# Optimization experiments

Hardware: AMD Instinct MI355X
Metric: run time of the kernel (lower is better)

Reference implementation:

```python
import jax, jax.numpy as jnp
import numpy as np

# norse LIF/LI defaults
DT = 1e-3
TAU_SYN_INV = 200.0
TAU_MEM_INV = 100.0
V_TH = 1.0
V_LEAK = 0.0
V_RESET = 0.0
ALPHA = 100.0  # SuperSpike surrogate slope ('super' method)
N_CLASSES = 10


@jax.custom_vjp
def spike(x):
    # heaviside forward, SuperSpike surrogate backward
    return (x > 0).astype(x.dtype)

def _spike_fwd(x):
    return spike(x), x

def _spike_bwd(x, g):
    return (g / (ALPHA * jnp.abs(x) + 1.0) ** 2,)

spike.defvjp(_spike_fwd, _spike_bwd)


def conv2d(x, w, b):
    y = jax.lax.conv_general_dilated(x, w, (1, 1), 'VALID',
                                     dimension_numbers=('NCHW', 'OIHW', 'NCHW'))
    return y + b[None, :, None, None]


def maxpool2(x):
    return jax.lax.reduce_window(x, -jnp.inf, jax.lax.max,
                                 (1, 1, 2, 2), (1, 1, 2, 2), 'VALID')


def lif_step(inp, v, i):
    # norse lif_feed_forward_step
    v_dec = v + DT * TAU_MEM_INV * ((V_LEAK - v) + i)
    i_dec = i * (1.0 - DT * TAU_SYN_INV)
    z = spike(v_dec - V_TH)
    v_new = (1.0 - z) * v_dec + z * V_RESET
    i_new = i_dec + inp
    return z, v_new, i_new


def setup_inputs() -> dict:
    key = jax.random.key(0)
    ks = jax.random.split(key, 9)
    T, B, C, H = 32, 32, 1, 64
    feats = 13 * 13 * 32  # 5408
    return {
        'x': jax.random.normal(ks[0], (T, B, C, H, H), jnp.float32),
        'conv1_w': jax.random.normal(ks[1], (16, 1, 5, 5), jnp.float32) * 0.2,
        'conv1_b': jax.random.normal(ks[2], (16,), jnp.float32) * 0.1,
        'conv2_w': jax.random.normal(ks[3], (32, 16, 5, 5), jnp.float32) * 0.05,
        'conv2_b': jax.random.normal(ks[4], (32,), jnp.float32) * 0.1,
        'fc1_w': jax.random.normal(ks[5], (500, feats), jnp.float32) * 0.02,
        'fc1_b': jax.random.normal(ks[6], (500,), jnp.float32) * 0.1,
        'out_w': jax.random.normal(ks[7], (10, 500), jnp.float32) * 0.06,
    }


def reference(x, conv1_w, conv1_b, conv2_w, conv2_b, fc1_w, fc1_b, out_w):
    B = x.shape[1]
    zeros = lambda s: jnp.zeros(s, x.dtype)
    init = ((zeros((B, 16, 60, 60)), zeros((B, 16, 60, 60))),
            (zeros((B, 32, 26, 26)), zeros((B, 32, 26, 26))),
            (zeros((B, 500)), zeros((B, 500))),
            (zeros((B, N_CLASSES)), zeros((B, N_CLASSES))))

    def step(state, xt):
        (v0, i0), (v1, i1), (v2, i2), (vo, io) = state
        z = conv2d(xt, conv1_w, conv1_b)                     # [B,16,60,60]
        z, v0, i0 = lif_step(z, v0, i0)
        z = maxpool2(z)                                      # [B,16,30,30]
        z = N_CLASSES * conv2d(z, conv2_w, conv2_b)          # [B,32,26,26]
        z, v1, i1 = lif_step(z, v1, i1)
        z = maxpool2(z).reshape(B, -1)                       # [B,5408]
        z = z @ fc1_w.T + fc1_b                              # [B,500]
        z, v2, i2 = lif_step(z, v2, i2)
        zr = jax.nn.relu(z)
        # LI (non-spiking) linear readout cell: norse li_step, no bias
        v_out = vo + DT * TAU_MEM_INV * ((V_LEAK - vo) + io)
        io = io * (1.0 - DT * TAU_SYN_INV) + zr @ out_w.T
        return ((v0, i0), (v1, i1), (v2, i2), (v_out, io)), v_out

    _, voltages = jax.lax.scan(step, init, x)
    return voltages  # [T, B, n_classes]
```

## Files before the change

kernel.cpp:

```cpp
#include <hip/hip_runtime.h>


#define T_STEPS 32

typedef __bf16 bf16x8 __attribute__((ext_vector_type(8)));
typedef float f32x16 __attribute__((ext_vector_type(16)));
typedef int i32x4 __attribute__((ext_vector_type(4)));

__device__ __forceinline__ int xcd_swz(int orig, int nwg) {
    const int q = nwg >> 3, r = nwg & 7;
    const int xcd = orig & 7, idx = orig >> 3;
    return (xcd < r ? xcd * (q + 1) : r * (q + 1) + (xcd - r) * q) + idx;
}

__global__ __launch_bounds__(256) void k_tr(
    const float* __restrict__ x, float* __restrict__ xT)
{
    const int y = blockIdx.x, t = blockIdx.y;
    const int tid = threadIdx.x;
    __shared__ float tile[32][65];

    const int lx = tid & 63, bg = tid >> 6;
    #pragma unroll
    for (int p = 0; p < 8; ++p) {
        const int b = bg + p * 4;
        tile[b][lx] = x[((size_t)(t * 32 + b) * 64 + y) * 64 + lx];
    }
    __syncthreads();
    const int wb = tid & 31, xg = tid >> 5;
    #pragma unroll
    for (int p = 0; p < 8; ++p) {
        const int xx = xg + p * 8;
        xT[((size_t)(t * 64 + y) * 64 + xx) * 32 + wb] = tile[wb][xx];
    }
}

__global__ __launch_bounds__(256) void k1_conv1(
    const float* __restrict__ xT,
    const float* __restrict__ w1,
    const float* __restrict__ b1,
    unsigned short* __restrict__ zp1c)
{
    const int pos = xcd_swz(blockIdx.x, 900);
    const int py = pos / 30, px = pos % 30;
    const int y0 = 2 * py, x0 = 2 * px;
    const int tid = threadIdx.x;
    const int b = tid & 31, slot = tid >> 5;

    __shared__ float ws[400];
    __shared__ float win[1152];
    for (int i = tid; i < 400; i += 256) ws[i] = w1[i];
    const float bias0 = b1[slot], bias1 = b1[slot + 8];
    const float* __restrict__ wc0 = ws + slot * 25;
    const float* __restrict__ wc1 = ws + (slot + 8) * 25;

    float v[2][4] = {{0.f,0.f,0.f,0.f},{0.f,0.f,0.f,0.f}};
    float cu[2][4] = {{0.f,0.f,0.f,0.f},{0.f,0.f,0.f,0.f}};

    const size_t obase = (size_t)pos * 256 + (slot >> 1) * 64 + b * 2 + (slot & 1);

    for (int t = 0; t < T_STEPS; ++t) {
        __syncthreads();
        {
            const float4* __restrict__ src0 =
                (const float4*)(xT + ((size_t)(t * 64 + y0) * 64 + x0) * 32);
            float4* __restrict__ dst = (float4*)win;
            for (int i = tid; i < 288; i += 256) {
                const int r = i / 48, j = i - r * 48;
                dst[r * 48 + j] = src0[r * 512 + j];
            }
        }
        __syncthreads();

        float xr[36];
        #pragma unroll
        for (int rc = 0; rc < 36; ++rc) xr[rc] = win[rc * 32 + b];

        float acc0[4] = {0.f, 0.f, 0.f, 0.f};
        float acc1[4] = {0.f, 0.f, 0.f, 0.f};
        #pragma unroll
        for (int ky = 0; ky < 5; ++ky) {
            #pragma unroll
            for (int kx = 0; kx < 5; ++kx) {
                const float w0 = wc0[ky * 5 + kx];
                const float w1v = wc1[ky * 5 + kx];
                const float e00 = xr[ky * 6 + kx];
                const float e01 = xr[ky * 6 + kx + 1];
                const float e10 = xr[(ky + 1) * 6 + kx];
                const float e11 = xr[(ky + 1) * 6 + kx + 1];
                acc0[0] = fmaf(w0, e00, acc0[0]);
                acc0[1] = fmaf(w0, e01, acc0[1]);
                acc0[2] = fmaf(w0, e10, acc0[2]);
                acc0[3] = fmaf(w0, e11, acc0[3]);
                acc1[0] = fmaf(w1v, e00, acc1[0]);
                acc1[1] = fmaf(w1v, e01, acc1[1]);
                acc1[2] = fmaf(w1v, e10, acc1[2]);
                acc1[3] = fmaf(w1v, e11, acc1[3]);
            }
        }

        #pragma unroll
        for (int half = 0; half < 2; ++half) {
            const float* acc = half ? acc1 : acc0;
            const float bias = half ? bias1 : bias0;
            float zmax = 0.f;
            #pragma unroll
            for (int q = 0; q < 4; ++q) {
                const float inp = acc[q] + bias;
                const float vv = v[half][q], cur = cu[half][q];
                const float vd = vv + 0.1f * (cur - vv);
                const float id = 0.8f * cur;
                const float z = (vd - 1.0f > 0.0f) ? 1.0f : 0.0f;
                v[half][q] = (z > 0.f) ? 0.f : vd;
                cu[half][q] = id + inp;
                zmax = fmaxf(zmax, z);
            }
            zp1c[(size_t)t * 460800 + (size_t)half * 230400 + obase] =
                (unsigned short)(__float_as_uint(zmax) >> 16);
        }
    }
}

__global__ __launch_bounds__(256) void k2w_split(
    const float* __restrict__ w2, unsigned short* __restrict__ wsplit)
{
    const int i = blockIdx.x * 256 + threadIdx.x;
    if (i >= 12800) return;
    const int co = i / 400, rest = i % 400;
    const int ci = rest / 25, tap = rest % 25;
    const float w = w2[i];
    const unsigned wb = __float_as_uint(w);
    const unsigned hi = wb & 0xFFFF0000u;
    const float r1 = w - __uint_as_float(hi);
    const unsigned mid = __float_as_uint(r1) & 0xFFFF0000u;
    const float r2 = r1 - __uint_as_float(mid);
    const unsigned lo = __float_as_uint(r2) & 0xFFFF0000u;
    const int base = (tap * 32 + co) * 16 + ci;
    wsplit[base]         = (unsigned short)(hi >> 16);
    wsplit[12800 + base] = (unsigned short)(mid >> 16);
    wsplit[25600 + base] = (unsigned short)(lo >> 16);
}

__global__ __launch_bounds__(256, 2) void k2a_mfma(
    const unsigned* __restrict__ zp1c,
    const unsigned short* __restrict__ wsplit,
    float* __restrict__ raw)
{
    __shared__ i32x4 wlds[4800];
    const int tid = threadIdx.x;
    for (int i = tid; i < 4800; i += 256)
        wlds[i] = ((const i32x4*)wsplit)[i];
    __syncthreads();

    const int w = tid >> 6, l = tid & 63;
    const int task = xcd_swz(blockIdx.x, 1352) * 4 + w;
    const int t = task / 169, pg = task % 169;
    const int py = pg / 13, px = pg % 13;
    const int b = l & 31, cig = l >> 5;
    const int abase = (l & 31) * 2 + cig;

    const unsigned* __restrict__ zt =
        zp1c + (size_t)(t * 2 + cig) * 115200 + ((2 * py) * 30 + 2 * px) * 128 + b;

    f32x16 accA, accB, accC, accD;
    #pragma unroll
    for (int r = 0; r < 16; ++r) { accA[r] = 0.f; accB[r] = 0.f; accC[r] = 0.f; accD[r] = 0.f; }

    #pragma unroll
    for (int wy = 0; wy < 6; ++wy) {
        i32x4 bw[6];
        #pragma unroll
        for (int wx = 0; wx < 6; ++wx) {
            const unsigned* __restrict__ c = zt + (wy * 30 + wx) * 128;
            bw[wx][0] = (int)c[0];
            bw[wx][1] = (int)c[32];
            bw[wx][2] = (int)c[64];
            bw[wx][3] = (int)c[96];
        }
        if (wy <= 4) {
            #pragma unroll
            for (int sp = 0; sp < 3; ++sp) {
                #pragma unroll
                for (int kx = 0; kx < 5; ++kx) {
                    const int tap = wy * 5 + kx;
                    const bf16x8 A = __builtin_bit_cast(bf16x8, wlds[(sp * 25 + tap) * 64 + abase]);
                    accA = __builtin_amdgcn_mfma_f32_32x32x16_bf16(
                        A, __builtin_bit_cast(bf16x8, bw[kx]),     accA, 0, 0, 0);
                    accB = __builtin_amdgcn_mfma_f32_32x32x16_bf16(
                        A, __builtin_bit_cast(bf16x8, bw[kx + 1]), accB, 0, 0, 0);
                }
            }
        }
        if (wy >= 1) {
            #pragma unroll
            for (int sp = 0; sp < 3; ++sp) {
                #pragma unroll
                for (int kx = 0; kx < 5; ++kx) {
                    const int tap = (wy - 1) * 5 + kx;
                    const bf16x8 A = __builtin_bit_cast(bf16x8, wlds[(sp * 25 + tap) * 64 + abase]);
                    accC = __builtin_amdgcn_mfma_f32_32x32x16_bf16(
                        A, __builtin_bit_cast(bf16x8, bw[kx]),     accC, 0, 0, 0);
                    accD = __builtin_amdgcn_mfma_f32_32x32x16_bf16(
                        A, __builtin_bit_cast(bf16x8, bw[kx + 1]), accD, 0, 0, 0);
                }
            }
        }
    }

    float* __restrict__ rp = raw + (size_t)(t * 169 + pg) * 4096 + b;
    const int hi = l >> 5;
    #pragma unroll
    for (int r = 0; r < 16; ++r) {
        const int row = (r & 3) + 8 * (r >> 2) + 4 * hi;
        rp[row * 32]        = accA[r];
        rp[1024 + row * 32] = accB[r];
        rp[2048 + row * 32] = accC[r];
        rp[3072 + row * 32] = accD[r];
    }
}

__global__ __launch_bounds__(256) void k2b_lifpool(
    const float* __restrict__ raw,
    const float* __restrict__ b2,
    float* __restrict__ zp2a)
{
    const int bid = blockIdx.x;
    const int pg = bid >> 2, cog = bid & 3;
    const int tid = threadIdx.x;
    const int co = cog * 8 + (tid >> 5), b = tid & 31;
    const float bias = b2[co];
    const float* __restrict__ rp = raw + (size_t)pg * 4096 + co * 32 + b;

    float v0=0.f,v1=0.f,v2=0.f,v3=0.f, c0=0.f,c1=0.f,c2=0.f,c3=0.f;
    for (int t = 0; t < T_STEPS; ++t) {
        const float* __restrict__ r = rp + (size_t)t * 692224;
        float zm = 0.f;
        { const float inp = 10.f*(r[0]    + bias); const float vd = v0 + 0.1f*(c0-v0);
          const float z = (vd-1.f>0.f)?1.f:0.f; v0 = (z>0.f)?0.f:vd; c0 = 0.8f*c0 + inp;
          zm = fmaxf(zm, z); }
        { const float inp = 10.f*(r[1024] + bias); const float vd = v1 + 0.1f*(c1-v1);
          const float z = (vd-1.f>0.f)?1.f:0.f; v1 = (z>0.f)?0.f:vd; c1 = 0.8f*c1 + inp;
          zm = fmaxf(zm, z); }
        { const float inp = 10.f*(r[2048] + bias); const float vd = v2 + 0.1f*(c2-v2);
          const float z = (vd-1.f>0.f)?1.f:0.f; v2 = (z>0.f)?0.f:vd; c2 = 0.8f*c2 + inp;
          zm = fmaxf(zm, z); }
        { const float inp = 10.f*(r[3072] + bias); const float vd = v3 + 0.1f*(c3-v3);
          const float z = (vd-1.f>0.f)?1.f:0.f; v3 = (z>0.f)?0.f:vd; c3 = 0.8f*c3 + inp;
          zm = fmaxf(zm, z); }
        zp2a[(size_t)t * 173056 + (co * 169 + pg) * 32 + b] = zm;
    }
}

__global__ __launch_bounds__(256) void k3w_split(
    const float* __restrict__ fw, unsigned short* __restrict__ wf)
{
    const int gid = blockIdx.x * 256 + threadIdx.x;
    const int l = gid & 31;
    const int ks = (gid >> 5) % 338;
    const int nt = gid / 10816;
    const int n = nt * 32 + l;

    unsigned hipk[8], midpk[8], lopk[8];
    #pragma unroll
    for (int p = 0; p < 8; ++p) {
        unsigned h[2], m[2], o[2];
        #pragma unroll
        for (int e = 0; e < 2; ++e) {
            const float w = (n < 500) ? fw[(size_t)n * 5408 + ks * 16 + 2 * p + e] : 0.f;
            const unsigned wb = __float_as_uint(w);
            const unsigned hi = wb & 0xFFFF0000u;
            const float r1 = w - __uint_as_float(hi);
            const unsigned mid = __float_as_uint(r1) & 0xFFFF0000u;
            const float r2 = r1 - __uint_as_float(mid);
            h[e] = hi >> 16; m[e] = mid >> 16; o[e] = __float_as_uint(r2) >> 16;
        }
        hipk[p]  = h[0] | (h[1] << 16);
        midpk[p] = m[0] | (m[1] << 16);
        lopk[p]  = o[0] | (o[1] << 16);
    }

    i32x4* __restrict__ wv = (i32x4*)wf;
    const int base = (nt * 338 + ks) * 64 + l * 2;
    i32x4 a, bq;
    a[0]=(int)hipk[0];a[1]=(int)hipk[1];a[2]=(int)hipk[2];a[3]=(int)hipk[3];
    bq[0]=(int)hipk[4];bq[1]=(int)hipk[5];bq[2]=(int)hipk[6];bq[3]=(int)hipk[7];
    wv[base] = a; wv[base + 1] = bq;
    a[0]=(int)midpk[0];a[1]=(int)midpk[1];a[2]=(int)midpk[2];a[3]=(int)midpk[3];
    bq[0]=(int)midpk[4];bq[1]=(int)midpk[5];bq[2]=(int)midpk[6];bq[3]=(int)midpk[7];
    wv[base + 346112] = a; wv[base + 346113] = bq;
    a[0]=(int)lopk[0];a[1]=(int)lopk[1];a[2]=(int)lopk[2];a[3]=(int)lopk[3];
    bq[0]=(int)lopk[4];bq[1]=(int)lopk[5];bq[2]=(int)lopk[6];bq[3]=(int)lopk[7];
    wv[base + 692224] = a; wv[base + 692225] = bq;
}

__global__ __launch_bounds__(256) void zpack(
    const float* __restrict__ zp2a, unsigned short* __restrict__ zb)
{
    const int gid = blockIdx.x * 256 + threadIdx.x;
    const int b = gid & 31;
    const int kh = (gid >> 5) & 1;
    const int rest = gid >> 6;
    const int ks = rest % 338;
    const int t = rest / 338;

    const float* __restrict__ zp = zp2a + (size_t)t * 173056 + (ks * 16 + kh * 8) * 32 + b;
    i32x4 pk;
    #pragma unroll
    for (int p = 0; p < 4; ++p) {
        const unsigned v0 = __float_as_uint(zp[(2 * p) * 32]) >> 16;
        const unsigned v1 = __float_as_uint(zp[(2 * p + 1) * 32]) & 0xFFFF0000u;
        pk[p] = (int)(v0 | v1);
    }
    ((i32x4*)zb)[gid] = pk;
}

__global__ __launch_bounds__(256) void k3_mfma(
    const unsigned short* __restrict__ wf,
    const unsigned short* __restrict__ zb,
    float* __restrict__ part)
{
    const int wgid = xcd_swz(blockIdx.x, 416);
    const int ntg = wgid / 52, rest = wgid % 52;
    const int kc = rest >> 2, cgg = rest & 3;
    const int tid = threadIdx.x;
    const int w = tid >> 6, l = tid & 63;
    const int nt = ntg * 2 + (w >> 1);
    const int cg = cgg * 2 + (w & 1);
    const int lo5 = l & 31, hi1 = l >> 5;

    const i32x4* __restrict__ wv = (const i32x4*)wf;
    const i32x4* __restrict__ zv = (const i32x4*)zb;

    f32x16 acc0, acc1, acc2, acc3;
    #pragma unroll
    for (int r = 0; r < 16; ++r) { acc0[r]=0.f; acc1[r]=0.f; acc2[r]=0.f; acc3[r]=0.f; }

    const int ks0 = kc * 26;
    #pragma unroll 2
    for (int kk = 0; kk < 26; ++kk) {
        const int ks = ks0 + kk;
        const int ab = (nt * 338 + ks) * 64 + lo5 * 2 + hi1;
        const bf16x8 A0 = __builtin_bit_cast(bf16x8, wv[ab]);
        const bf16x8 A1 = __builtin_bit_cast(bf16x8, wv[ab + 346112]);
        const bf16x8 A2 = __builtin_bit_cast(bf16x8, wv[ab + 692224]);
        const int b0 = (((cg * 4) * 338 + ks) * 2 + hi1) * 32 + lo5;
        const bf16x8 B0 = __builtin_bit_cast(bf16x8, zv[b0]);
        const bf16x8 B1 = __builtin_bit_cast(bf16x8, zv[b0 + 21632]);
        const bf16x8 B2 = __builtin_bit_cast(bf16x8, zv[b0 + 43264]);
        const bf16x8 B3 = __builtin_bit_cast(bf16x8, zv[b0 + 64896]);
        acc0 = __builtin_amdgcn_mfma_f32_32x32x16_bf16(A0, B0, acc0, 0, 0, 0);
        acc1 = __builtin_amdgcn_mfma_f32_32x32x16_bf16(A0, B1, acc1, 0, 0, 0);
        acc2 = __builtin_amdgcn_mfma_f32_32x32x16_bf16(A0, B2, acc2, 0, 0, 0);
        acc3 = __builtin_amdgcn_mfma_f32_32x32x16_bf16(A0, B3, acc3, 0, 0, 0);
        acc0 = __builtin_amdgcn_mfma_f32_32x32x16_bf16(A1, B0, acc0, 0, 0, 0);
        acc1 = __builtin_amdgcn_mfma_f32_32x32x16_bf16(A1, B1, acc1, 0, 0, 0);
        acc2 = __builtin_amdgcn_mfma_f32_32x32x16_bf16(A1, B2, acc2, 0, 0, 0);
        acc3 = __builtin_amdgcn_mfma_f32_32x32x16_bf16(A1, B3, acc3, 0, 0, 0);
        acc0 = __builtin_amdgcn_mfma_f32_32x32x16_bf16(A2, B0, acc0, 0, 0, 0);
        acc1 = __builtin_amdgcn_mfma_f32_32x32x16_bf16(A2, B1, acc1, 0, 0, 0);
        acc2 = __builtin_amdgcn_mfma_f32_32x32x16_bf16(A2, B2, acc2, 0, 0, 0);
        acc3 = __builtin_amdgcn_mfma_f32_32x32x16_bf16(A2, B3, acc3, 0, 0, 0);
    }

    float* __restrict__ pp = part + ((size_t)(kc * 512 + nt * 32)) * 1024 + cg * 128 + lo5;
    #pragma unroll
    for (int r = 0; r < 16; ++r) {
        const int row = (r & 3) + 8 * (r >> 2) + 4 * hi1;
        pp[row * 1024]      = acc0[r];
        pp[row * 1024 + 32] = acc1[r];
        pp[row * 1024 + 64] = acc2[r];
        pp[row * 1024 + 96] = acc3[r];
    }
}

__global__ __launch_bounds__(256) void k3b_lif(
    const float* __restrict__ part,
    const float* __restrict__ fb,
    float* __restrict__ za)
{
    const int idx = blockIdx.x * 256 + threadIdx.x;
    if (idx >= 16000) return;
    const int n = idx >> 5, b = idx & 31;
    const float bias = fb[n];

    float v = 0.f, cu = 0.f;
    for (int t = 0; t < T_STEPS; ++t) {
        float s = 0.f;
        #pragma unroll
        for (int p = 0; p < 13; ++p)
            s += part[(size_t)p * 524288 + n * 1024 + t * 32 + b];
        s += bias;

        const float vd = v + 0.1f * (cu - v);
        const float id = 0.8f * cu;
        const float z = (vd - 1.0f > 0.0f) ? 1.0f : 0.0f;
        v = (z > 0.f) ? 0.f : vd;
        cu = id + s;
        za[(size_t)t * 16000 + idx] = z;
    }
}

__global__ __launch_bounds__(256) void k4_dot(
    const float* __restrict__ za,
    const float* __restrict__ ow,
    float* __restrict__ dota)
{
    const int c = blockIdx.x, t = blockIdx.y;
    const int tid = threadIdx.x;
    const int b = tid & 31, nc = tid >> 5;
    const float* __restrict__ wr = ow + c * 500;
    const float* __restrict__ zt = za + (size_t)t * 16000;

    float acc = 0.f;
    for (int j = 0; j < 63; ++j) {
        const int n = nc * 63 + j;
        if (n < 500) acc = fmaf(zt[n * 32 + b], wr[n], acc);
    }

    __shared__ float red[256];
    red[tid] = acc;
    __syncthreads();
    if (tid < 32) {
        float dot = 0.f;
        #pragma unroll
        for (int q = 0; q < 8; ++q) dot += red[q * 32 + tid];
        dota[((size_t)t * 10 + c) * 32 + tid] = dot;
    }
}

__global__ __launch_bounds__(320) void k5_li(
    const float* __restrict__ dota,
    float* __restrict__ outp)
{
    const int tid = threadIdx.x;
    if (tid >= 320) return;
    const int c = tid / 32, b = tid & 31;

    float vo = 0.f, io = 0.f;
    for (int t = 0; t < T_STEPS; ++t) {
        const float vout = vo + 0.1f * (io - vo);
        outp[t * 320 + b * 10 + c] = vout;
        vo = vout;
        io = 0.8f * io + dota[(t * 10 + c) * 32 + b];
    }
}

extern "C" void kernel_launch(void* const* d_in, const int* in_sizes, int n_in,
                              void* d_out, int out_size, void* d_ws, size_t ws_size,
                              hipStream_t stream) {
    const float* x  = (const float*)d_in[0];
    const float* w1 = (const float*)d_in[1];
    const float* b1 = (const float*)d_in[2];
    const float* w2 = (const float*)d_in[3];
    const float* b2 = (const float*)d_in[4];
    const float* fw = (const float*)d_in[5];
    const float* fb = (const float*)d_in[6];
    const float* ow = (const float*)d_in[7];
    float* out = (float*)d_out;
    float* ws = (float*)d_ws;

    size_t off = 0;
    float* zp1a = ws + off; off += 14745600;
    float* zp2a = ws + off; off += 5537792;
    float* za   = ws + off; off += 512000;
    float* dota = ws + off; off += 10240;
    unsigned short* wsplit = (unsigned short*)(ws + off); off += 19200;
    float* big  = ws + off; off += 22151168;

    float* xT       = big;
    float* conv2raw = big;
    float* part     = big;
    unsigned short* zp1c = (unsigned short*)zp1a;
    unsigned short* zb = (unsigned short*)zp1a;
    unsigned short* wf = (unsigned short*)(zp1a + 4194304);

    k2w_split<<<50, 256, 0, stream>>>(w2, wsplit);
    k_tr     <<<dim3(64, 32), 256, 0, stream>>>(x, xT);
    k1_conv1 <<<900, 256, 0, stream>>>(xT, w1, b1, zp1c);
    k2a_mfma <<<1352, 256, 0, stream>>>((const unsigned*)zp1c, wsplit, conv2raw);
    k2b_lifpool<<<676, 256, 0, stream>>>(conv2raw, b2, zp2a);
    k3w_split<<<676, 256, 0, stream>>>(fw, wf);
    zpack    <<<2704, 256, 0, stream>>>(zp2a, zb);
    k3_mfma  <<<416, 256, 0, stream>>>(wf, zb, part);
    k3b_lif  <<<63, 256, 0, stream>>>(part, fb, za);
    k4_dot   <<<dim3(10, 32), 256, 0, stream>>>(za, ow, dota);
    k5_li    <<<1, 320, 0, stream>>>(dota, out);
}
```

Before: 236.2 us.

## Batch conv1 timesteps in LDS, keep weights in registers, fuse zpack into lifpool

conv1 now loads an 8-timestep input window into shared memory at once, stored in a transposed per-batch layout so that float4 reads can be used. This cuts the number of barriers per block from 64 to 8. Filter weights are held in registers instead of shared memory. The separate zpack kernel is removed: k2b_lifpool writes bf16 spikes directly in the packed layout that k3_mfma expects, which avoids one launch and an fp32 intermediate round trip. The trade-off is more registers and LDS per block in conv1, plus scattered 2-byte stores in lifpool.

```diff
diff --git a/kernel.cpp b/kernel.cpp
--- a/kernel.cpp
+++ b/kernel.cpp
@@ -47,76 +47,97 @@
     const int tid = threadIdx.x;
     const int b = tid & 31, slot = tid >> 5;
 
-    __shared__ float ws[400];
-    __shared__ float win[1152];
-    for (int i = tid; i < 400; i += 256) ws[i] = w1[i];
+    __shared__ float win[8 * 32 * 36];
+
+    float wreg[2][25];
+    #pragma unroll
+    for (int k = 0; k < 25; ++k) {
+        wreg[0][k] = w1[slot * 25 + k];
+        wreg[1][k] = w1[(slot + 8) * 25 + k];
+    }
     const float bias0 = b1[slot], bias1 = b1[slot + 8];
-    const float* __restrict__ wc0 = ws + slot * 25;
-    const float* __restrict__ wc1 = ws + (slot + 8) * 25;
 
     float v[2][4] = {{0.f,0.f,0.f,0.f},{0.f,0.f,0.f,0.f}};
     float cu[2][4] = {{0.f,0.f,0.f,0.f},{0.f,0.f,0.f,0.f}};
 
     const size_t obase = (size_t)pos * 256 + (slot >> 1) * 64 + b * 2 + (slot & 1);
 
-    for (int t = 0; t < T_STEPS; ++t) {
+    for (int tp = 0; tp < 4; ++tp) {
         __syncthreads();
-        {
-            const float4* __restrict__ src0 =
-                (const float4*)(xT + ((size_t)(t * 64 + y0) * 64 + x0) * 32);
-            float4* __restrict__ dst = (float4*)win;
-            for (int i = tid; i < 288; i += 256) {
-                const int r = i / 48, j = i - r * 48;
-                dst[r * 48 + j] = src0[r * 512 + j];
+        for (int i = tid; i < 2304; i += 256) {
+            const int tt = i >> 8;
+            const int tt2 = i / 288;
+            const int rem = i - tt2 * 288;
+            const int r = rem / 48, j = rem - r * 48;
+            const int xoff = j >> 3, b0 = (j & 7) * 4;
+            (void)tt;
+            const float4 val = *(const float4*)(xT +
+                ((size_t)((tp * 8 + tt2) * 64 + y0 + r) * 64 + (x0 + xoff)) * 32 + b0);
+            const int rc = r * 6 + xoff;
+            float* __restrict__ wp = win + (tt2 * 32 + b0) * 36 + rc;
+            wp[0]   = val.x;
+            wp[36]  = val.y;
+            wp[72]  = val.z;
+            wp[108] = val.w;
+        }
+        __syncthreads();
+
+        for (int tt = 0; tt < 8; ++tt) {
+            const int t = tp * 8 + tt;
+            const float* __restrict__ myrow = win + (tt * 32 + b) * 36;
+            float xr[36];
+            #pragma unroll
+            for (int q4 = 0; q4 < 9; ++q4) {
+                const float4 u = *(const float4*)(myrow + q4 * 4);
+                xr[q4 * 4]     = u.x;
+                xr[q4 * 4 + 1] = u.y;
+                xr[q4 * 4 + 2] = u.z;
+                xr[q4 * 4 + 3] = u.w;
             }
-        }
-        __syncthreads();
-
-        float xr[36];
-        #pragma unroll
-        for (int rc = 0; rc < 36; ++rc) xr[rc] = win[rc * 32 + b];
-
-        float acc0[4] = {0.f, 0.f, 0.f, 0.f};
-        float acc1[4] = {0.f, 0.f, 0.f, 0.f};
-        #pragma unroll
-        for (int ky = 0; ky < 5; ++ky) {
+
+            float acc0[4] = {0.f, 0.f, 0.f, 0.f};
+            float acc1[4] = {0.f, 0.f, 0.f, 0.f};
             #pragma unroll
-            for (int kx = 0; kx < 5; ++kx) {
-                const float w0 = wc0[ky * 5 + kx];
-                const float w1v = wc1[ky * 5 + kx];
-                const float e00 = xr[ky * 6 + kx];
-                const float e01 = xr[ky * 6 + kx + 1];
-                const float e10 = xr[(ky + 1) * 6 + kx];
-                const float e11 = xr[(ky + 1) * 6 + kx + 1];
-                acc0[0] = fmaf(w0, e00, acc0[0]);
-                acc0[1] = fmaf(w0, e01, acc0[1]);
-                acc0[2] = fmaf(w0, e10, acc0[2]);
-                acc0[3] = fmaf(w0, e11, acc0[3]);
-                acc1[0] = fmaf(w1v, e00, acc1[0]);
-                acc1[1] = fmaf(w1v, e01, acc1[1]);
-                acc1[2] = fmaf(w1v, e10, acc1[2]);
-                acc1[3] = fmaf(w1v, e11, acc1[3]);
+            for (int ky = 0; ky < 5; ++ky) {
+                #pragma unroll
+                for (int kx = 0; kx < 5; ++kx) {
+                    const int tap = ky * 5 + kx;
+                    const float e00 = xr[ky * 6 + kx];
+                    const float e01 = xr[ky * 6 + kx + 1];
+                    const float e10 = xr[(ky + 1) * 6 + kx];
+                    const float e11 = xr[(ky + 1) * 6 + kx + 1];
+                    const float w0 = wreg[0][tap];
+                    acc0[0] = fmaf(w0, e00, acc0[0]);
+                    acc0[1] = fmaf(w0, e01, acc0[1]);
+                    acc0[2] = fmaf(w0, e10, acc0[2]);
+                    acc0[3] = fmaf(w0, e11, acc0[3]);
+                    const float w1v = wreg[1][tap];
+                    acc1[0] = fmaf(w1v, e00, acc1[0]);
+                    acc1[1] = fmaf(w1v, e01, acc1[1]);
+                    acc1[2] = fmaf(w1v, e10, acc1[2]);
+                    acc1[3] = fmaf(w1v, e11, acc1[3]);
+                }
             }
-        }
-
-        #pragma unroll
-        for (int half = 0; half < 2; ++half) {
-            const float* acc = half ? acc1 : acc0;
-            const float bias = half ? bias1 : bias0;
-            float zmax = 0.f;
+
             #pragma unroll
-            for (int q = 0; q < 4; ++q) {
-                const float inp = acc[q] + bias;
-                const float vv = v[half][q], cur = cu[half][q];
-                const float vd = vv + 0.1f * (cur - vv);
-                const float id = 0.8f * cur;
-                const float z = (vd - 1.0f > 0.0f) ? 1.0f : 0.0f;
-                v[half][q] = (z > 0.f) ? 0.f : vd;
-                cu[half][q] = id + inp;
-                zmax = fmaxf(zmax, z);
+            for (int half = 0; half < 2; ++half) {
+                const float* acc = half ? acc1 : acc0;
+                const float bias = half ? bias1 : bias0;
+                float zmax = 0.f;
+                #pragma unroll
+                for (int q = 0; q < 4; ++q) {
+                    const float inp = acc[q] + bias;
+                    const float vv = v[half][q], curr = cu[half][q];
+                    const float vd = vv + 0.1f * (curr - vv);
+                    const float id = 0.8f * curr;
+                    const float z = (vd - 1.0f > 0.0f) ? 1.0f : 0.0f;
+                    v[half][q] = (z > 0.f) ? 0.f : vd;
+                    cu[half][q] = id + inp;
+                    zmax = fmaxf(zmax, z);
+                }
+                zp1c[(size_t)t * 460800 + (size_t)half * 230400 + obase] =
+                    (unsigned short)(__float_as_uint(zmax) >> 16);
             }
-            zp1c[(size_t)t * 460800 + (size_t)half * 230400 + obase] =
-                (unsigned short)(__float_as_uint(zmax) >> 16);
         }
     }
 }
@@ -222,7 +243,7 @@
 __global__ __launch_bounds__(256) void k2b_lifpool(
     const float* __restrict__ raw,
     const float* __restrict__ b2,
-    float* __restrict__ zp2a)
+    unsigned short* __restrict__ zb)
 {
     const int bid = blockIdx.x;
     const int pg = bid >> 2, cog = bid & 3;
@@ -230,6 +251,9 @@
     const int co = cog * 8 + (tid >> 5), b = tid & 31;
     const float bias = b2[co];
     const float* __restrict__ rp = raw + (size_t)pg * 4096 + co * 32 + b;
+
+    const int k = co * 169 + pg;
+    const size_t zidx0 = ((size_t)((k >> 4) * 2 + ((k >> 3) & 1)) * 32 + b) * 8 + (k & 7);
 
     float v0=0.f,v1=0.f,v2=0.f,v3=0.f, c0=0.f,c1=0.f,c2=0.f,c3=0.f;
     for (int t = 0; t < T_STEPS; ++t) {
@@ -247,7 +271,8 @@
         { const float inp = 10.f*(r[3072] + bias); const float vd = v3 + 0.1f*(c3-v3);
           const float z = (vd-1.f>0.f)?1.f:0.f; v3 = (z>0.f)?0.f:vd; c3 = 0.8f*c3 + inp;
           zm = fmaxf(zm, z); }
-        zp2a[(size_t)t * 173056 + (co * 169 + pg) * 32 + b] = zm;
+        zb[(size_t)t * 173056 + zidx0] =
+            (unsigned short)(__float_as_uint(zm) >> 16);
     }
 }
 
@@ -291,27 +316,6 @@
     a[0]=(int)lopk[0];a[1]=(int)lopk[1];a[2]=(int)lopk[2];a[3]=(int)lopk[3];
     bq[0]=(int)lopk[4];bq[1]=(int)lopk[5];bq[2]=(int)lopk[6];bq[3]=(int)lopk[7];
     wv[base + 692224] = a; wv[base + 692225] = bq;
-}
-
-__global__ __launch_bounds__(256) void zpack(
-    const float* __restrict__ zp2a, unsigned short* __restrict__ zb)
-{
-    const int gid = blockIdx.x * 256 + threadIdx.x;
-    const int b = gid & 31;
-    const int kh = (gid >> 5) & 1;
-    const int rest = gid >> 6;
-    const int ks = rest % 338;
-    const int t = rest / 338;
-
-    const float* __restrict__ zp = zp2a + (size_t)t * 173056 + (ks * 16 + kh * 8) * 32 + b;
-    i32x4 pk;
-    #pragma unroll
-    for (int p = 0; p < 4; ++p) {
-        const unsigned v0 = __float_as_uint(zp[(2 * p) * 32]) >> 16;
-        const unsigned v1 = __float_as_uint(zp[(2 * p + 1) * 32]) & 0xFFFF0000u;
-        pk[p] = (int)(v0 | v1);
-    }
-    ((i32x4*)zb)[gid] = pk;
 }
 
 __global__ __launch_bounds__(256) void k3_mfma(
@@ -461,7 +465,6 @@
 
     size_t off = 0;
     float* zp1a = ws + off; off += 14745600;
-    float* zp2a = ws + off; off += 5537792;
     float* za   = ws + off; off += 512000;
     float* dota = ws + off; off += 10240;
     unsigned short* wsplit = (unsigned short*)(ws + off); off += 19200;
@@ -470,17 +473,16 @@
     float* xT       = big;
     float* conv2raw = big;
     float* part     = big;
-    unsigned short* zp1c = (unsigned short*)zp1a;
+    unsigned short* zp1c16 = (unsigned short*)zp1a;
     unsigned short* zb = (unsigned short*)zp1a;
     unsigned short* wf = (unsigned short*)(zp1a + 4194304);
 
     k2w_split<<<50, 256, 0, stream>>>(w2, wsplit);
     k_tr     <<<dim3(64, 32), 256, 0, stream>>>(x, xT);
-    k1_conv1 <<<900, 256, 0, stream>>>(xT, w1, b1, zp1c);
-    k2a_mfma <<<1352, 256, 0, stream>>>((const unsigned*)zp1c, wsplit, conv2raw);
-    k2b_lifpool<<<676, 256, 0, stream>>>(conv2raw, b2, zp2a);
+    k1_conv1 <<<900, 256, 0, stream>>>(xT, w1, b1, zp1c16);
+    k2a_mfma <<<1352, 256, 0, stream>>>((const unsigned*)zp1c16, wsplit, conv2raw);
+    k2b_lifpool<<<676, 256, 0, stream>>>(conv2raw, b2, zb);
     k3w_split<<<676, 256, 0, stream>>>(fw, wf);
-    zpack    <<<2704, 256, 0, stream>>>(zp2a, zb);
     k3_mfma  <<<416, 256, 0, stream>>>(wf, zb, part);
     k3b_lif  <<<63, 256, 0, stream>>>(part, fb, za);
     k4_dot   <<<dim3(10, 32), 256, 0, stream>>>(za, ow, dota);
```

Measured after the change: 241.0 us. +2.1%, slower.
